# Kernel optimization log

Measured on AMD Instinct MI355X. Metric: run time of the kernel, lower is better.

The kernel has to match this reference:

```python
import jax, jax.numpy as jnp
import numpy as np

T, B, E, H, V = 512, 64, 512, 1024, 256


def setup_inputs() -> dict:
    key = jax.random.key(0)
    ks = jax.random.split(key, 10)
    s = lambda k, shape, sc: jax.random.normal(k, shape, dtype=jnp.float32) * sc
    return {
        "ints": jax.random.randint(ks[0], (T, B), 0, V),
        "encodings": s(ks[1], (V, E), 1.0),
        "output0": s(ks[2], (H,), 1.0),
        "memory0": s(ks[3], (H,), 1.0),
        "W_ih": s(ks[4], (4 * H, E), 0.03),
        "W_hh": s(ks[5], (4 * H, H), 0.03),
        "b_ih": s(ks[6], (4 * H,), 0.03),
        "b_hh": s(ks[7], (4 * H,), 0.03),
        "W_dec": s(ks[8], (V, H), 0.03),
        "b_dec": jnp.zeros((V,), dtype=jnp.float32),
    }


def reference(ints, encodings, output0, memory0, W_ih, W_hh, b_ih, b_hh, W_dec, b_dec):
    t, b = ints.shape
    h = output0.shape[0]
    x = encodings[ints]                                   # [T,B,E] embedding gather
    h0 = jnp.broadcast_to(output0, (b, h))                # learned initial hidden
    c0 = jnp.broadcast_to(memory0, (b, h))                # learned initial cell
    # precompute input projection for all timesteps (one big GEMM)
    x_proj = jnp.einsum('tbe,ge->tbg', x, W_ih) + b_ih + b_hh  # [T,B,4H]

    def step(carry, xp):
        hh, cc = carry
        gates = xp + hh @ W_hh.T                          # [B,4H]
        i, f, g, o = jnp.split(gates, 4, axis=-1)         # torch gate order i,f,g,o
        i = jax.nn.sigmoid(i)
        f = jax.nn.sigmoid(f)
        g = jnp.tanh(g)
        o = jax.nn.sigmoid(o)
        cc = f * cc + i * g
        hh = o * jnp.tanh(cc)
        return (hh, cc), hh

    _, hs = jax.lax.scan(step, (h0, c0), x_proj)          # [T,B,H]
    # outputs shifted right by one: predict char t from state after chars <t
    outs = jnp.concatenate([h0[None], hs[:-1]], axis=0)   # [T,B,H]
    return outs @ W_dec.T + b_dec                          # [T,B,V]
```

## Files before the change

kernel.cpp:

```cpp
#include <hip/hip_runtime.h>


#define TT 512
#define BB 64
#define HH 1024
#define VV 256
#define EE 512
#define SPIN_CAP 16384

typedef __attribute__((ext_vector_type(8))) short bf16x8;
typedef __attribute__((ext_vector_type(4))) float f32x4;
typedef __attribute__((ext_vector_type(4))) int i32x4;
typedef __attribute__((ext_vector_type(4))) unsigned short u16x4;

static __device__ __forceinline__ unsigned short f2bf(float f) {
  union { float f; unsigned u; } x; x.f = f;
  unsigned r = x.u + 0x7fffu + ((x.u >> 16) & 1u);
  return (unsigned short)(r >> 16);
}

__global__ void cvt_bf16(const float* __restrict__ s, unsigned short* __restrict__ d, int n4) {
  int i = blockIdx.x * blockDim.x + threadIdx.x;
  int st = gridDim.x * blockDim.x;
  for (; i < n4; i += st) {
    f32x4 v = *(const f32x4*)(s + 4l * i);
    u16x4 o;
    o.x = f2bf(v.x); o.y = f2bf(v.y); o.z = f2bf(v.z); o.w = f2bf(v.w);
    *(u16x4*)(d + 4l * i) = o;
  }
}

__global__ __launch_bounds__(256) void proj_kernel(
    const unsigned short* __restrict__ A,
    const unsigned short* __restrict__ Wi,
    const float* __restrict__ bih, const float* __restrict__ bhh,
    float* __restrict__ proj)
{
  __shared__ __align__(16) unsigned char Asm[64 * 128];
  const int tid = threadIdx.x;
  const int w = tid >> 6;
  const int lane = tid & 63;
  const int ln = lane & 15, kg = lane >> 4;
  const int m0 = blockIdx.x * 64;
  const int nb = blockIdx.y * 256 + w * 64;
  const int srow = tid >> 2, skq = tid & 3;

  f32x4 acc[4][4];
  for (int a = 0; a < 4; ++a) for (int b = 0; b < 4; ++b) acc[a][b] = (f32x4){0.f,0.f,0.f,0.f};

  for (int kc = 0; kc < 8; ++kc) {
    {
      const unsigned short* src = A + (m0 + srow) * 512 + kc * 64 + skq * 16;
      unsigned base = (unsigned)(srow * 128 + skq * 32);
      unsigned sw = (unsigned)((srow & 7) << 4);
      *(i32x4*)(Asm + ((base) ^ sw))      = *(const i32x4*)(src);
      *(i32x4*)(Asm + ((base + 16) ^ sw)) = *(const i32x4*)(src + 8);
    }
    __syncthreads();
    for (int kk = 0; kk < 2; ++kk) {
      bf16x8 afr[4];
      for (int mi = 0; mi < 4; ++mi) {
        int row = mi * 16 + ln;
        unsigned off = (unsigned)(row * 128 + (kk * 32 + kg * 8) * 2);
        afr[mi] = *(const bf16x8*)(Asm + (off ^ ((unsigned)(row & 7) << 4)));
      }
      for (int ni = 0; ni < 4; ++ni) {
        const unsigned short* bp = Wi + (nb + ni * 16 + ln) * 512 + kc * 64 + kk * 32 + kg * 8;
        bf16x8 bfr = *(const bf16x8*)bp;
        for (int mi = 0; mi < 4; ++mi)
          acc[mi][ni] = __builtin_amdgcn_mfma_f32_16x16x32_bf16(afr[mi], bfr, acc[mi][ni], 0, 0, 0);
      }
    }
    __syncthreads();
  }
  for (int ni = 0; ni < 4; ++ni) {
    int nn = nb + ni * 16 + ln;
    int gi = nn >> 10, uu = nn & 1023;
    float bias = bih[nn] + bhh[nn];
    for (int mi = 0; mi < 4; ++mi) {
      int mr = m0 + mi * 16 + kg * 4;
      for (int r = 0; r < 4; ++r)
        proj[(size_t)(mr + r) * 4096 + uu * 4 + gi] = acc[mi][ni][r] + bias;
    }
  }
}

__global__ __launch_bounds__(512, 2) void scan_kernel(
    const unsigned short* __restrict__ Whh,
    const float* __restrict__ proj,
    const int* __restrict__ ints,
    const float* __restrict__ h0v,
    const float* __restrict__ c0v,
    unsigned int* __restrict__ hcomm,
    unsigned short* __restrict__ outs)
{
  __shared__ float gatesm[8 * 8 * 128];

  const int tid = threadIdx.x;
  const int blk = blockIdx.x;
  const int g = blk & 7, r = blk >> 3;
  const int w = tid >> 6, lane = tid & 63;
  const int ln = lane & 15, kg = lane >> 4;
  const int s = (tid & 255) >> 5, u = tid & 31;
  const int sg = g * 8 + s;
  const int ug = r * 32 + u;

  bf16x8 bw[8][4];
#pragma unroll
  for (int nt = 0; nt < 8; ++nt) {
    int lrow = nt * 16 + ln;
    int grow = (lrow >> 5) * 1024 + r * 32 + (lrow & 31);
    const unsigned short* wp = Whh + (size_t)grow * 1024 + w * 128 + kg * 8;
#pragma unroll
    for (int kt = 0; kt < 4; ++kt)
      bw[nt][kt] = *(const bf16x8*)(wp + kt * 32);
  }
#pragma unroll
  for (int nt = 0; nt < 8; ++nt)
#pragma unroll
    for (int kt = 0; kt < 4; ++kt)
      asm volatile("" : "+v"(bw[nt][kt]));

  float c = (tid < 256) ? c0v[ug] : 0.f;

  if (tid < 256) {
    unsigned short hb = f2bf(h0v[ug]);
    unsigned word = ((unsigned)hb << 16) | 1u;
    unsigned* hp = hcomm + 65536 + (size_t)sg * 1024 + ug;
    asm volatile("global_store_dword %0, %1, off sc0 sc1" :: "v"(hp), "v"(word) : "memory");
    outs[(size_t)sg * 1024 + ug] = hb;
  }

  i32x4 q[8];
#pragma unroll
  for (int i = 0; i < 8; ++i) q[i] = (i32x4){0, 0, 0, 0};

  for (int t = 0; t < TT - 1; ++t) {
    f32x4 prv = (f32x4){0.f,0.f,0.f,0.f};
    if (tid < 256) {
      int vocab = ints[t * 64 + sg];
      const float* pp = proj + (size_t)vocab * 4096 + ug * 4;
      asm volatile("global_load_dwordx4 %0, %1, off" : "=v"(prv) : "v"(pp) : "memory");
    }

    const unsigned* ab = hcomm + ((size_t)((t + 1) & 1)) * 65536
                       + (size_t)(g * 8 + (ln & 7)) * 1024 + w * 128 + kg * 8;
    unsigned tgt = (unsigned)(t + 1);
    {
      int guard = 0;
      while (true) {
        if (ln < 8) {
#define LQ(i, off_lit) \
          asm volatile("global_load_dwordx4 %0, %1, off offset:" off_lit " sc0 sc1" \
                       : "=v"(q[i]) : "v"(ab) : "memory")
          LQ(0, "0");   LQ(1, "16");  LQ(2, "128"); LQ(3, "144");
          LQ(4, "256"); LQ(5, "272"); LQ(6, "384"); LQ(7, "400");
#undef LQ
        }
        asm volatile("s_waitcnt vmcnt(0)" ::: "memory");
        __builtin_amdgcn_sched_barrier(0);
        unsigned bad = 0;
        if (ln < 8) {
#pragma unroll
          for (int i = 0; i < 8; ++i) {
            bad |= ((unsigned)q[i].x ^ tgt);
            bad |= ((unsigned)q[i].y ^ tgt);
            bad |= ((unsigned)q[i].z ^ tgt);
            bad |= ((unsigned)q[i].w ^ tgt);
          }
        }
        if (__all(ln >= 8 || (bad & 0xffffu) == 0u)) break;
        if (++guard > SPIN_CAP) break;
      }
    }
    __builtin_amdgcn_sched_barrier(0);

    f32x4 acc[8];
#pragma unroll
    for (int i = 0; i < 8; ++i) acc[i] = (f32x4){0.f,0.f,0.f,0.f};
#pragma unroll
    for (int kt = 0; kt < 4; ++kt) {
      i32x4 lo = q[2 * kt], hi = q[2 * kt + 1];
      unsigned d0 = ((unsigned)lo.x >> 16) | ((unsigned)lo.y & 0xffff0000u);
      unsigned d1 = ((unsigned)lo.z >> 16) | ((unsigned)lo.w & 0xffff0000u);
      unsigned d2 = ((unsigned)hi.x >> 16) | ((unsigned)hi.y & 0xffff0000u);
      unsigned d3 = ((unsigned)hi.z >> 16) | ((unsigned)hi.w & 0xffff0000u);
      union { i32x4 i; bf16x8 h; } u2;
      u2.i = (i32x4){ (int)d0, (int)d1, (int)d2, (int)d3 };
#pragma unroll
      for (int nt = 0; nt < 8; ++nt)
        acc[nt] = __builtin_amdgcn_mfma_f32_16x16x32_bf16(u2.h, bw[nt][kt], acc[nt], 0, 0, 0);
    }

#pragma unroll
    for (int nt = 0; nt < 8; ++nt) {
      if (kg < 2) {
#pragma unroll
        for (int rr = 0; rr < 4; ++rr)
          gatesm[(w * 8 + kg * 4 + rr) * 128 + nt * 16 + ln] = acc[nt][rr];
      }
    }
    __syncthreads();

    if (tid < 256) {
      float g0 = prv.x, g1 = prv.y, g2 = prv.z, g3 = prv.w;
#pragma unroll
      for (int ww = 0; ww < 8; ++ww) {
        const float* gm = gatesm + (ww * 8 + s) * 128 + u;
        g0 += gm[0];
        g1 += gm[32];
        g2 += gm[64];
        g3 += gm[96];
      }
      float ii = __builtin_amdgcn_rcpf(1.f + __expf(-g0));
      float ff = __builtin_amdgcn_rcpf(1.f + __expf(-g1));
      float gt = 1.f - 2.f * __builtin_amdgcn_rcpf(1.f + __expf(2.f * g2));
      float oo = __builtin_amdgcn_rcpf(1.f + __expf(-g3));
      c = ff * c + ii * gt;
      float hv = oo * (1.f - 2.f * __builtin_amdgcn_rcpf(1.f + __expf(2.f * c)));

      unsigned short hb = f2bf(hv);
      unsigned word = ((unsigned)hb << 16) | ((unsigned)(t + 2) & 0xffffu);
      unsigned* hp = hcomm + ((size_t)((t + 2) & 1)) * 65536 + (size_t)sg * 1024 + ug;
      asm volatile("global_store_dword %0, %1, off sc0 sc1" :: "v"(hp), "v"(word) : "memory");
      outs[(size_t)(t + 1) * 65536 + (size_t)sg * 1024 + ug] = hb;
    }
    __syncthreads();
  }
}

__global__ __launch_bounds__(256) void decode_kernel(
    const unsigned short* __restrict__ A,
    const unsigned short* __restrict__ Wd,
    const float* __restrict__ bdec,
    float* __restrict__ out)
{
  __shared__ __align__(16) unsigned char Asm[64 * 128];
  const int tid = threadIdx.x;
  const int w = tid >> 6;
  const int lane = tid & 63;
  const int ln = lane & 15, kg = lane >> 4;
  const int m0 = blockIdx.x * 64;
  const int nb = w * 64;
  const int srow = tid >> 2, skq = tid & 3;

  f32x4 acc[4][4];
  for (int a = 0; a < 4; ++a) for (int b = 0; b < 4; ++b) acc[a][b] = (f32x4){0.f,0.f,0.f,0.f};

  for (int kc = 0; kc < 16; ++kc) {
    {
      const unsigned short* src = A + (m0 + srow) * 1024 + kc * 64 + skq * 16;
      unsigned base = (unsigned)(srow * 128 + skq * 32);
      unsigned sw = (unsigned)((srow & 7) << 4);
      *(i32x4*)(Asm + ((base) ^ sw))      = *(const i32x4*)(src);
      *(i32x4*)(Asm + ((base + 16) ^ sw)) = *(const i32x4*)(src + 8);
    }
    __syncthreads();
    for (int kk = 0; kk < 2; ++kk) {
      bf16x8 afr[4];
      for (int mi = 0; mi < 4; ++mi) {
        int row = mi * 16 + ln;
        unsigned off = (unsigned)(row * 128 + (kk * 32 + kg * 8) * 2);
        afr[mi] = *(const bf16x8*)(Asm + (off ^ ((unsigned)(row & 7) << 4)));
      }
      for (int ni = 0; ni < 4; ++ni) {
        const unsigned short* bp = Wd + (nb + ni * 16 + ln) * 1024 + kc * 64 + kk * 32 + kg * 8;
        bf16x8 bfr = *(const bf16x8*)bp;
        for (int mi = 0; mi < 4; ++mi)
          acc[mi][ni] = __builtin_amdgcn_mfma_f32_16x16x32_bf16(afr[mi], bfr, acc[mi][ni], 0, 0, 0);
      }
    }
    __syncthreads();
  }
  for (int ni = 0; ni < 4; ++ni) {
    int nn = nb + ni * 16 + ln;
    float bd = bdec[nn];
    for (int mi = 0; mi < 4; ++mi) {
      int mr = m0 + mi * 16 + kg * 4;
      for (int r = 0; r < 4; ++r)
        out[(mr + r) * 256 + nn] = acc[mi][ni][r] + bd;
    }
  }
}

extern "C" void kernel_launch(void* const* d_in, const int* in_sizes, int n_in,
                              void* d_out, int out_size, void* d_ws, size_t ws_size,
                              hipStream_t stream) {
  const int*   ints = (const int*)  d_in[0];
  const float* enc  = (const float*)d_in[1];
  const float* out0 = (const float*)d_in[2];
  const float* mem0 = (const float*)d_in[3];
  const float* Wih  = (const float*)d_in[4];
  const float* Whh  = (const float*)d_in[5];
  const float* bih  = (const float*)d_in[6];
  const float* bhh  = (const float*)d_in[7];
  const float* Wdec = (const float*)d_in[8];
  const float* bdec = (const float*)d_in[9];
  float* out = (float*)d_out;

  char* ws = (char*)d_ws;
  size_t off = 0;
  auto alloc = [&](size_t bytes) { char* p = ws + off; off += (bytes + 255) & ~(size_t)255; return p; };
  unsigned short* Whh_bf  = (unsigned short*)alloc(4096ull * 1024 * 2);
  unsigned short* enc_bf  = (unsigned short*)alloc(256ull * 512 * 2);
  unsigned short* Wih_bf  = (unsigned short*)alloc(4096ull * 512 * 2);
  unsigned short* Wdec_bf = (unsigned short*)alloc(256ull * 1024 * 2);
  float*          proj    = (float*)alloc(256ull * 4096 * 4);
  unsigned short* outs_bf = (unsigned short*)alloc(512ull * 64 * 1024 * 2);
  unsigned int*   hcomm   = (unsigned int*)alloc(2ull * 64 * 1024 * 4);

  hipMemsetAsync(hcomm, 0, 2ull * 64 * 1024 * 4, stream);

  cvt_bf16<<<512, 256, 0, stream>>>(Whh,  Whh_bf,  4096 * 1024 / 4);
  cvt_bf16<<<64,  256, 0, stream>>>(enc,  enc_bf,  256 * 512 / 4);
  cvt_bf16<<<256, 256, 0, stream>>>(Wih,  Wih_bf,  4096 * 512 / 4);
  cvt_bf16<<<64,  256, 0, stream>>>(Wdec, Wdec_bf, 256 * 1024 / 4);

  proj_kernel<<<dim3(4, 16), 256, 0, stream>>>(enc_bf, Wih_bf, bih, bhh, proj);

  {
    const unsigned short* a0 = Whh_bf;
    const float* a1 = proj;
    const int* a2 = ints;
    const float* a3 = out0;
    const float* a4 = mem0;
    unsigned int* a5 = hcomm;
    unsigned short* a6 = outs_bf;
    void* args[] = { &a0, &a1, &a2, &a3, &a4, &a5, &a6 };
    hipError_t e = hipLaunchCooperativeKernel((const void*)scan_kernel,
                                              dim3(256), dim3(512), args, 0, stream);
    if (e != hipSuccess) {
      scan_kernel<<<256, 512, 0, stream>>>(Whh_bf, proj, ints, out0, mem0,
                                           hcomm, outs_bf);
    }
  }

  decode_kernel<<<512, 256, 0, stream>>>(outs_bf, Wdec_bf, bdec, out);
}
```

Before: 1.710 ms.

## Replace per-element tagged handoff with per-step group counters and direct bf16 reads

Each block now publishes its new hidden state as plain bf16 directly into the outs buffer, then bumps a per-timestep, per-batch-group atomic counter. Consumers spin on a single counter until it reaches 32 producers, instead of polling 16-bit tags packed into every hidden element. After that they load the bf16 rows directly as MFMA operands, so the unpacking work goes away. The next step's projection load is prefetched early and the W_hh fragments are hinted into AGPRs. In exchange, each step adds a store drain and a barrier before the atomic, a second round trip after the flag, and a lower spin cap that raises the risk of silent early exits.

```diff
diff --git a/kernel.cpp b/kernel.cpp
--- a/kernel.cpp
+++ b/kernel.cpp
@@ -6,7 +6,7 @@
 #define HH 1024
 #define VV 256
 #define EE 512
-#define SPIN_CAP 16384
+#define SPIN_CAP 4096
 
 typedef __attribute__((ext_vector_type(8))) short bf16x8;
 typedef __attribute__((ext_vector_type(4))) float f32x4;
@@ -91,7 +91,7 @@
     const int* __restrict__ ints,
     const float* __restrict__ h0v,
     const float* __restrict__ c0v,
-    unsigned int* __restrict__ hcomm,
+    unsigned int* __restrict__ cnt,
     unsigned short* __restrict__ outs)
 {
   __shared__ float gatesm[8 * 8 * 128];
@@ -119,78 +119,56 @@
   for (int nt = 0; nt < 8; ++nt)
 #pragma unroll
     for (int kt = 0; kt < 4; ++kt)
-      asm volatile("" : "+v"(bw[nt][kt]));
+      asm volatile("" : "+a"(bw[nt][kt]));
 
   float c = (tid < 256) ? c0v[ug] : 0.f;
 
   if (tid < 256) {
     unsigned short hb = f2bf(h0v[ug]);
-    unsigned word = ((unsigned)hb << 16) | 1u;
-    unsigned* hp = hcomm + 65536 + (size_t)sg * 1024 + ug;
-    asm volatile("global_store_dword %0, %1, off sc0 sc1" :: "v"(hp), "v"(word) : "memory");
-    outs[(size_t)sg * 1024 + ug] = hb;
-  }
-
-  i32x4 q[8];
-#pragma unroll
-  for (int i = 0; i < 8; ++i) q[i] = (i32x4){0, 0, 0, 0};
+    unsigned short* hp = outs + (size_t)sg * 1024 + ug;
+    asm volatile("global_store_short %0, %1, off sc0 sc1" :: "v"(hp), "v"((unsigned)hb) : "memory");
+  }
+  asm volatile("s_waitcnt vmcnt(0)" ::: "memory");
+  __syncthreads();
+  if (tid == 0)
+    __hip_atomic_fetch_add(&cnt[g], 1u, __ATOMIC_RELAXED, __HIP_MEMORY_SCOPE_AGENT);
+
+  f32x4 prv = (f32x4){0.f,0.f,0.f,0.f};
+  if (tid < 256) {
+    int vocab = ints[sg];
+    prv = *(const f32x4*)(proj + (size_t)vocab * 4096 + ug * 4);
+  }
 
   for (int t = 0; t < TT - 1; ++t) {
-    f32x4 prv = (f32x4){0.f,0.f,0.f,0.f};
-    if (tid < 256) {
-      int vocab = ints[t * 64 + sg];
-      const float* pp = proj + (size_t)vocab * 4096 + ug * 4;
-      asm volatile("global_load_dwordx4 %0, %1, off" : "=v"(prv) : "v"(pp) : "memory");
-    }
-
-    const unsigned* ab = hcomm + ((size_t)((t + 1) & 1)) * 65536
-                       + (size_t)(g * 8 + (ln & 7)) * 1024 + w * 128 + kg * 8;
-    unsigned tgt = (unsigned)(t + 1);
     {
       int guard = 0;
-      while (true) {
-        if (ln < 8) {
-#define LQ(i, off_lit) \
-          asm volatile("global_load_dwordx4 %0, %1, off offset:" off_lit " sc0 sc1" \
-                       : "=v"(q[i]) : "v"(ab) : "memory")
-          LQ(0, "0");   LQ(1, "16");  LQ(2, "128"); LQ(3, "144");
-          LQ(4, "256"); LQ(5, "272"); LQ(6, "384"); LQ(7, "400");
-#undef LQ
-        }
-        asm volatile("s_waitcnt vmcnt(0)" ::: "memory");
-        __builtin_amdgcn_sched_barrier(0);
-        unsigned bad = 0;
-        if (ln < 8) {
-#pragma unroll
-          for (int i = 0; i < 8; ++i) {
-            bad |= ((unsigned)q[i].x ^ tgt);
-            bad |= ((unsigned)q[i].y ^ tgt);
-            bad |= ((unsigned)q[i].z ^ tgt);
-            bad |= ((unsigned)q[i].w ^ tgt);
-          }
-        }
-        if (__all(ln >= 8 || (bad & 0xffffu) == 0u)) break;
+      while (__hip_atomic_load(&cnt[t * 8 + g], __ATOMIC_RELAXED, __HIP_MEMORY_SCOPE_AGENT) < 32u) {
         if (++guard > SPIN_CAP) break;
       }
     }
     __builtin_amdgcn_sched_barrier(0);
 
+    bf16x8 av[4];
+    {
+      const unsigned short* ab = outs + (size_t)(t * 64 + g * 8 + (ln & 7)) * 1024
+                               + w * 128 + kg * 8;
+#define LA(i, off_lit) \
+      asm volatile("global_load_dwordx4 %0, %1, off offset:" off_lit " sc0 sc1" \
+                   : "=v"(av[i]) : "v"(ab) : "memory")
+      LA(0, "0"); LA(1, "64"); LA(2, "128"); LA(3, "192");
+#undef LA
+      asm volatile("s_waitcnt vmcnt(0)" ::: "memory");
+      __builtin_amdgcn_sched_barrier(0);
+    }
+
     f32x4 acc[8];
 #pragma unroll
     for (int i = 0; i < 8; ++i) acc[i] = (f32x4){0.f,0.f,0.f,0.f};
 #pragma unroll
-    for (int kt = 0; kt < 4; ++kt) {
-      i32x4 lo = q[2 * kt], hi = q[2 * kt + 1];
-      unsigned d0 = ((unsigned)lo.x >> 16) | ((unsigned)lo.y & 0xffff0000u);
-      unsigned d1 = ((unsigned)lo.z >> 16) | ((unsigned)lo.w & 0xffff0000u);
-      unsigned d2 = ((unsigned)hi.x >> 16) | ((unsigned)hi.y & 0xffff0000u);
-      unsigned d3 = ((unsigned)hi.z >> 16) | ((unsigned)hi.w & 0xffff0000u);
-      union { i32x4 i; bf16x8 h; } u2;
-      u2.i = (i32x4){ (int)d0, (int)d1, (int)d2, (int)d3 };
+    for (int kt = 0; kt < 4; ++kt)
 #pragma unroll
       for (int nt = 0; nt < 8; ++nt)
-        acc[nt] = __builtin_amdgcn_mfma_f32_16x16x32_bf16(u2.h, bw[nt][kt], acc[nt], 0, 0, 0);
-    }
+        acc[nt] = __builtin_amdgcn_mfma_f32_16x16x32_bf16(av[kt], bw[nt][kt], acc[nt], 0, 0, 0);
 
 #pragma unroll
     for (int nt = 0; nt < 8; ++nt) {
@@ -220,12 +198,18 @@
       float hv = oo * (1.f - 2.f * __builtin_amdgcn_rcpf(1.f + __expf(2.f * c)));
 
       unsigned short hb = f2bf(hv);
-      unsigned word = ((unsigned)hb << 16) | ((unsigned)(t + 2) & 0xffffu);
-      unsigned* hp = hcomm + ((size_t)((t + 2) & 1)) * 65536 + (size_t)sg * 1024 + ug;
-      asm volatile("global_store_dword %0, %1, off sc0 sc1" :: "v"(hp), "v"(word) : "memory");
-      outs[(size_t)(t + 1) * 65536 + (size_t)sg * 1024 + ug] = hb;
-    }
-    __syncthreads();
+      unsigned short* hp = outs + (size_t)((t + 1) * 64 + sg) * 1024 + ug;
+      asm volatile("global_store_short %0, %1, off sc0 sc1" :: "v"(hp), "v"((unsigned)hb) : "memory");
+
+      if (t + 1 < TT - 1) {
+        int vocab = ints[(t + 1) * 64 + sg];
+        prv = *(const f32x4*)(proj + (size_t)vocab * 4096 + ug * 4);
+      }
+    }
+    asm volatile("s_waitcnt vmcnt(0)" ::: "memory");
+    __syncthreads();
+    if (tid == 0)
+      __hip_atomic_fetch_add(&cnt[(t + 1) * 8 + g], 1u, __ATOMIC_RELAXED, __HIP_MEMORY_SCOPE_AGENT);
   }
 }
 
@@ -307,9 +291,9 @@
   unsigned short* Wdec_bf = (unsigned short*)alloc(256ull * 1024 * 2);
   float*          proj    = (float*)alloc(256ull * 4096 * 4);
   unsigned short* outs_bf = (unsigned short*)alloc(512ull * 64 * 1024 * 2);
-  unsigned int*   hcomm   = (unsigned int*)alloc(2ull * 64 * 1024 * 4);
-
-  hipMemsetAsync(hcomm, 0, 2ull * 64 * 1024 * 4, stream);
+  unsigned int*   cnt     = (unsigned int*)alloc(512ull * 8 * 4);
+
+  hipMemsetAsync(cnt, 0, 512ull * 8 * 4, stream);
 
   cvt_bf16<<<512, 256, 0, stream>>>(Whh,  Whh_bf,  4096 * 1024 / 4);
   cvt_bf16<<<64,  256, 0, stream>>>(enc,  enc_bf,  256 * 512 / 4);
@@ -324,14 +308,14 @@
     const int* a2 = ints;
     const float* a3 = out0;
     const float* a4 = mem0;
-    unsigned int* a5 = hcomm;
+    unsigned int* a5 = cnt;
     unsigned short* a6 = outs_bf;
     void* args[] = { &a0, &a1, &a2, &a3, &a4, &a5, &a6 };
     hipError_t e = hipLaunchCooperativeKernel((const void*)scan_kernel,
                                               dim3(256), dim3(512), args, 0, stream);
     if (e != hipSuccess) {
       scan_kernel<<<256, 512, 0, stream>>>(Whh_bf, proj, ints, out0, mem0,
-                                           hcomm, outs_bf);
+                                           cnt, outs_bf);
     }
   }
 
```

Measured after the change: 2.358 ms. +37.9%, slower.

## Remap scan blocks by XCD and use L2-local flags for intra-group sync

Applied to the files above, without the earlier changes.

Each block reads its hardware XCC ID and takes a rank within that die, so each 8-sequence group g is served by blocks on a single XCD. A rehearsal handshake then runs a number of steps using sc0-only (non-system-scope) flag loads and stores. If all 32 blocks of a group complete it without hitting the spin cap, the main scan uses L2-local sc0 accesses instead of sc0 sc1 for the hidden-state exchange. This aims to cut inter-step synchronization latency, at the cost of the startup rehearsal and reliance on hardware block placement. The W_hh fragment register pin also changes from VGPR to AGPR.

```diff
diff --git a/kernel.cpp b/kernel.cpp
--- a/kernel.cpp
+++ b/kernel.cpp
@@ -7,6 +7,8 @@
 #define VV 256
 #define EE 512
 #define SPIN_CAP 16384
+#define REH_STEPS 48
+#define REH_CAP 4096
 
 typedef __attribute__((ext_vector_type(8))) short bf16x8;
 typedef __attribute__((ext_vector_type(4))) float f32x4;
@@ -85,41 +87,18 @@
   }
 }
 
-__global__ __launch_bounds__(512, 2) void scan_kernel(
-    const unsigned short* __restrict__ Whh,
-    const float* __restrict__ proj,
-    const int* __restrict__ ints,
-    const float* __restrict__ h0v,
-    const float* __restrict__ c0v,
-    unsigned int* __restrict__ hcomm,
-    unsigned short* __restrict__ outs)
+template<bool LOCAL>
+static __device__ __forceinline__ void scan_loop(
+    int g, int r, int tid, bf16x8 (&bw)[8][4],
+    const float* __restrict__ proj, const int* __restrict__ ints,
+    const float* __restrict__ h0v, const float* __restrict__ c0v,
+    unsigned int* __restrict__ hcomm, unsigned short* __restrict__ outs,
+    float* gatesm)
 {
-  __shared__ float gatesm[8 * 8 * 128];
-
-  const int tid = threadIdx.x;
-  const int blk = blockIdx.x;
-  const int g = blk & 7, r = blk >> 3;
   const int w = tid >> 6, lane = tid & 63;
   const int ln = lane & 15, kg = lane >> 4;
   const int s = (tid & 255) >> 5, u = tid & 31;
-  const int sg = g * 8 + s;
-  const int ug = r * 32 + u;
-
-  bf16x8 bw[8][4];
-#pragma unroll
-  for (int nt = 0; nt < 8; ++nt) {
-    int lrow = nt * 16 + ln;
-    int grow = (lrow >> 5) * 1024 + r * 32 + (lrow & 31);
-    const unsigned short* wp = Whh + (size_t)grow * 1024 + w * 128 + kg * 8;
-#pragma unroll
-    for (int kt = 0; kt < 4; ++kt)
-      bw[nt][kt] = *(const bf16x8*)(wp + kt * 32);
-  }
-#pragma unroll
-  for (int nt = 0; nt < 8; ++nt)
-#pragma unroll
-    for (int kt = 0; kt < 4; ++kt)
-      asm volatile("" : "+v"(bw[nt][kt]));
+  const int sg = g * 8 + s, ug = r * 32 + u;
 
   float c = (tid < 256) ? c0v[ug] : 0.f;
 
@@ -127,7 +106,8 @@
     unsigned short hb = f2bf(h0v[ug]);
     unsigned word = ((unsigned)hb << 16) | 1u;
     unsigned* hp = hcomm + 65536 + (size_t)sg * 1024 + ug;
-    asm volatile("global_store_dword %0, %1, off sc0 sc1" :: "v"(hp), "v"(word) : "memory");
+    if (LOCAL) asm volatile("global_store_dword %0, %1, off sc0"     :: "v"(hp), "v"(word) : "memory");
+    else       asm volatile("global_store_dword %0, %1, off sc0 sc1" :: "v"(hp), "v"(word) : "memory");
     outs[(size_t)sg * 1024 + ug] = hb;
   }
 
@@ -150,12 +130,21 @@
       int guard = 0;
       while (true) {
         if (ln < 8) {
-#define LQ(i, off_lit) \
+#define LQL(i, off_lit) \
+          asm volatile("global_load_dwordx4 %0, %1, off offset:" off_lit " sc0" \
+                       : "=v"(q[i]) : "v"(ab) : "memory")
+#define LQG(i, off_lit) \
           asm volatile("global_load_dwordx4 %0, %1, off offset:" off_lit " sc0 sc1" \
                        : "=v"(q[i]) : "v"(ab) : "memory")
-          LQ(0, "0");   LQ(1, "16");  LQ(2, "128"); LQ(3, "144");
-          LQ(4, "256"); LQ(5, "272"); LQ(6, "384"); LQ(7, "400");
-#undef LQ
+          if (LOCAL) {
+            LQL(0, "0");   LQL(1, "16");  LQL(2, "128"); LQL(3, "144");
+            LQL(4, "256"); LQL(5, "272"); LQL(6, "384"); LQL(7, "400");
+          } else {
+            LQG(0, "0");   LQG(1, "16");  LQG(2, "128"); LQG(3, "144");
+            LQG(4, "256"); LQG(5, "272"); LQG(6, "384"); LQG(7, "400");
+          }
+#undef LQL
+#undef LQG
         }
         asm volatile("s_waitcnt vmcnt(0)" ::: "memory");
         __builtin_amdgcn_sched_barrier(0);
@@ -222,11 +211,170 @@
       unsigned short hb = f2bf(hv);
       unsigned word = ((unsigned)hb << 16) | ((unsigned)(t + 2) & 0xffffu);
       unsigned* hp = hcomm + ((size_t)((t + 2) & 1)) * 65536 + (size_t)sg * 1024 + ug;
-      asm volatile("global_store_dword %0, %1, off sc0 sc1" :: "v"(hp), "v"(word) : "memory");
+      if (LOCAL) asm volatile("global_store_dword %0, %1, off sc0"     :: "v"(hp), "v"(word) : "memory");
+      else       asm volatile("global_store_dword %0, %1, off sc0 sc1" :: "v"(hp), "v"(word) : "memory");
       outs[(size_t)(t + 1) * 65536 + (size_t)sg * 1024 + ug] = hb;
     }
     __syncthreads();
   }
+}
+
+__global__ __launch_bounds__(512, 2) void scan_kernel(
+    const unsigned short* __restrict__ Whh,
+    const float* __restrict__ proj,
+    const int* __restrict__ ints,
+    const float* __restrict__ h0v,
+    const float* __restrict__ c0v,
+    unsigned int* __restrict__ hcomm,
+    unsigned int* __restrict__ rhbuf,
+    unsigned int* __restrict__ ctrl,
+    unsigned short* __restrict__ outs)
+{
+  __shared__ float gatesm[8 * 8 * 128];
+  __shared__ int s_g, s_r, s_bal, s_fail, s_mode;
+
+  const int tid = threadIdx.x;
+  const int blk = blockIdx.x;
+
+  if (tid == 0) {
+    unsigned xcd;
+    asm volatile("s_getreg_b32 %0, hwreg(HW_REG_XCC_ID)" : "=s"(xcd));
+    xcd &= 7u;
+    unsigned rank = __hip_atomic_fetch_add(&ctrl[xcd], 1u, __ATOMIC_RELAXED,
+                                           __HIP_MEMORY_SCOPE_AGENT);
+    __hip_atomic_fetch_add(&ctrl[8], 1u, __ATOMIC_RELEASE, __HIP_MEMORY_SCOPE_AGENT);
+    int guard = 0;
+    while (__hip_atomic_load(&ctrl[8], __ATOMIC_ACQUIRE, __HIP_MEMORY_SCOPE_AGENT) < 256u)
+      if (++guard > (1 << 20)) break;
+    unsigned bal = (rank < 32u) ? 1u : 0u;
+    for (int k = 0; k < 8; ++k)
+      bal &= (__hip_atomic_load(&ctrl[k], __ATOMIC_RELAXED, __HIP_MEMORY_SCOPE_AGENT) == 32u)
+             ? 1u : 0u;
+    s_bal = (int)bal;
+    s_g = bal ? (int)xcd  : (blk & 7);
+    s_r = bal ? (int)rank : (blk >> 3);
+    s_fail = 0;
+    s_mode = 0;
+  }
+  __syncthreads();
+  const int g = s_g, r = s_r;
+  const int w = tid >> 6, lane = tid & 63;
+  const int ln = lane & 15, kg = lane >> 4;
+  const int s = (tid & 255) >> 5, u = tid & 31;
+  const int sg = g * 8 + s, ug = r * 32 + u;
+
+  bf16x8 bw[8][4];
+#pragma unroll
+  for (int nt = 0; nt < 8; ++nt) {
+    int lrow = nt * 16 + ln;
+    int grow = (lrow >> 5) * 1024 + r * 32 + (lrow & 31);
+    const unsigned short* wp = Whh + (size_t)grow * 1024 + w * 128 + kg * 8;
+#pragma unroll
+    for (int kt = 0; kt < 4; ++kt)
+      bw[nt][kt] = *(const bf16x8*)(wp + kt * 32);
+  }
+#pragma unroll
+  for (int nt = 0; nt < 8; ++nt)
+#pragma unroll
+    for (int kt = 0; kt < 4; ++kt)
+      asm volatile("" : "+a"(bw[nt][kt]));
+
+  if (s_bal) {
+    if (tid < 256) {
+      unsigned* p0 = rhbuf + (size_t)sg * 1024 + ug;
+      unsigned* p1 = rhbuf + 65536 + (size_t)sg * 1024 + ug;
+      unsigned z = 0;
+      asm volatile("global_store_dword %0, %1, off sc0" :: "v"(p0), "v"(z) : "memory");
+      asm volatile("global_store_dword %0, %1, off sc0" :: "v"(p1), "v"(z) : "memory");
+    }
+    asm volatile("s_waitcnt vmcnt(0)" ::: "memory");
+    __syncthreads();
+    if (tid < 256) {
+      unsigned word = 1u;
+      unsigned* hp = rhbuf + 65536 + (size_t)sg * 1024 + ug;
+      asm volatile("global_store_dword %0, %1, off sc0" :: "v"(hp), "v"(word) : "memory");
+    }
+    for (int t = 0; t < REH_STEPS - 1; ++t) {
+      const unsigned* ab = rhbuf + ((size_t)((t + 1) & 1)) * 65536
+                         + (size_t)(g * 8 + (ln & 7)) * 1024 + w * 128 + kg * 8;
+      unsigned tgt = (unsigned)(t + 1);
+      i32x4 q2[8];
+#pragma unroll
+      for (int i = 0; i < 8; ++i) q2[i] = (i32x4){0, 0, 0, 0};
+      int already = __hip_atomic_load(&s_fail, __ATOMIC_RELAXED, __HIP_MEMORY_SCOPE_WORKGROUP);
+      if (!already) {
+        int guard = 0;
+        while (true) {
+          if (ln < 8) {
+#define LR(i, off_lit) \
+            asm volatile("global_load_dwordx4 %0, %1, off offset:" off_lit " sc0" \
+                         : "=v"(q2[i]) : "v"(ab) : "memory")
+            LR(0, "0");   LR(1, "16");  LR(2, "128"); LR(3, "144");
+            LR(4, "256"); LR(5, "272"); LR(6, "384"); LR(7, "400");
+#undef LR
+          }
+          asm volatile("s_waitcnt vmcnt(0)" ::: "memory");
+          __builtin_amdgcn_sched_barrier(0);
+          unsigned bad = 0;
+          if (ln < 8) {
+#pragma unroll
+            for (int i = 0; i < 8; ++i) {
+              bad |= ((unsigned)q2[i].x ^ tgt);
+              bad |= ((unsigned)q2[i].y ^ tgt);
+              bad |= ((unsigned)q2[i].z ^ tgt);
+              bad |= ((unsigned)q2[i].w ^ tgt);
+            }
+          }
+          if (__all(ln >= 8 || (bad & 0xffffu) == 0u)) break;
+          if (++guard > REH_CAP) {
+            if (lane == 0)
+              __hip_atomic_store(&s_fail, 1, __ATOMIC_RELAXED, __HIP_MEMORY_SCOPE_WORKGROUP);
+            break;
+          }
+        }
+      }
+      __syncthreads();
+      if (tid < 256) {
+        unsigned word = (unsigned)(t + 2);
+        unsigned* hp = rhbuf + ((size_t)((t + 2) & 1)) * 65536 + (size_t)sg * 1024 + ug;
+        asm volatile("global_store_dword %0, %1, off sc0" :: "v"(hp), "v"(word) : "memory");
+      }
+      __syncthreads();
+    }
+    __syncthreads();
+
+    if (tid < 256) {
+      unsigned* p0 = hcomm + (size_t)sg * 1024 + ug;
+      unsigned* p1 = hcomm + 65536 + (size_t)sg * 1024 + ug;
+      unsigned z = 0;
+      asm volatile("global_store_dword %0, %1, off sc0" :: "v"(p0), "v"(z) : "memory");
+      asm volatile("global_store_dword %0, %1, off sc0" :: "v"(p1), "v"(z) : "memory");
+    }
+    asm volatile("s_waitcnt vmcnt(0)" ::: "memory");
+    __syncthreads();
+
+    int ok = (__hip_atomic_load(&s_fail, __ATOMIC_RELAXED, __HIP_MEMORY_SCOPE_WORKGROUP) == 0);
+    if (tid == 0)
+      __hip_atomic_store(&ctrl[16 + g * 32 + r], ok ? 2u : 1u,
+                         __ATOMIC_RELAXED, __HIP_MEMORY_SCOPE_AGENT);
+    if (tid == 0) s_mode = 1;
+    __syncthreads();
+    if (tid < 32) {
+      unsigned v = 0;
+      int guard = 0;
+      while ((v = __hip_atomic_load(&ctrl[16 + g * 32 + tid], __ATOMIC_RELAXED,
+                                    __HIP_MEMORY_SCOPE_AGENT)) == 0u)
+        if (++guard > (1 << 20)) break;
+      if (v != 2u)
+        __hip_atomic_store(&s_mode, 0, __ATOMIC_RELAXED, __HIP_MEMORY_SCOPE_WORKGROUP);
+    }
+    __syncthreads();
+  }
+
+  if (s_mode)
+    scan_loop<true >(g, r, tid, bw, proj, ints, h0v, c0v, hcomm, outs, gatesm);
+  else
+    scan_loop<false>(g, r, tid, bw, proj, ints, h0v, c0v, hcomm, outs, gatesm);
 }
 
 __global__ __launch_bounds__(256) void decode_kernel(
@@ -308,8 +456,10 @@
   float*          proj    = (float*)alloc(256ull * 4096 * 4);
   unsigned short* outs_bf = (unsigned short*)alloc(512ull * 64 * 1024 * 2);
   unsigned int*   hcomm   = (unsigned int*)alloc(2ull * 64 * 1024 * 4);
-
-  hipMemsetAsync(hcomm, 0, 2ull * 64 * 1024 * 4, stream);
+  unsigned int*   rhbuf   = (unsigned int*)alloc(2ull * 64 * 1024 * 4);
+  unsigned int*   ctrl    = (unsigned int*)alloc(272 * 4);
+
+  hipMemsetAsync(hcomm, 0, 2ull * (2ull * 64 * 1024 * 4 + 256) + 272 * 4, stream);
 
   cvt_bf16<<<512, 256, 0, stream>>>(Whh,  Whh_bf,  4096 * 1024 / 4);
   cvt_bf16<<<64,  256, 0, stream>>>(enc,  enc_bf,  256 * 512 / 4);
@@ -325,13 +475,15 @@
     const float* a3 = out0;
     const float* a4 = mem0;
     unsigned int* a5 = hcomm;
-    unsigned short* a6 = outs_bf;
-    void* args[] = { &a0, &a1, &a2, &a3, &a4, &a5, &a6 };
+    unsigned int* a6 = rhbuf;
+    unsigned int* a7 = ctrl;
+    unsigned short* a8 = outs_bf;
+    void* args[] = { &a0, &a1, &a2, &a3, &a4, &a5, &a6, &a7, &a8 };
     hipError_t e = hipLaunchCooperativeKernel((const void*)scan_kernel,
                                               dim3(256), dim3(512), args, 0, stream);
     if (e != hipSuccess) {
       scan_kernel<<<256, 512, 0, stream>>>(Whh_bf, proj, ints, out0, mem0,
-                                           hcomm, outs_bf);
+                                           hcomm, rhbuf, ctrl, outs_bf);
     }
   }
 
```

New measurement: 6.259 ms. 3.66x slower.

## Poll hidden-state chunks per k-tile and double-buffer gate smem to drop barrier

Applied to the files above, without the earlier changes.

The spin-wait on the flag-tagged hidden-state buffer is split into four per-k-tile polls, so MFMA work on early chunks can start before the whole slice is ready. The gate scratch buffer in LDS is double-buffered by timestep parity, which lets the trailing __syncthreads per step be removed. The register-resident W_hh fragments are also pinned to AGPRs to ease VGPR pressure. The costs are more polling round trips per step and twice the LDS footprint, which may reduce occupancy.

```diff
diff --git a/kernel.cpp b/kernel.cpp
--- a/kernel.cpp
+++ b/kernel.cpp
@@ -94,7 +94,7 @@
     unsigned int* __restrict__ hcomm,
     unsigned short* __restrict__ outs)
 {
-  __shared__ float gatesm[8 * 8 * 128];
+  __shared__ float gatesm[2 * 8 * 8 * 128];
 
   const int tid = threadIdx.x;
   const int blk = blockIdx.x;
@@ -119,7 +119,7 @@
   for (int nt = 0; nt < 8; ++nt)
 #pragma unroll
     for (int kt = 0; kt < 4; ++kt)
-      asm volatile("" : "+v"(bw[nt][kt]));
+      asm volatile("" : "+a"(bw[nt][kt]));
 
   float c = (tid < 256) ? c0v[ug] : 0.f;
 
@@ -131,10 +131,6 @@
     outs[(size_t)sg * 1024 + ug] = hb;
   }
 
-  i32x4 q[8];
-#pragma unroll
-  for (int i = 0; i < 8; ++i) q[i] = (i32x4){0, 0, 0, 0};
-
   for (int t = 0; t < TT - 1; ++t) {
     f32x4 prv = (f32x4){0.f,0.f,0.f,0.f};
     if (tid < 256) {
@@ -146,45 +142,41 @@
     const unsigned* ab = hcomm + ((size_t)((t + 1) & 1)) * 65536
                        + (size_t)(g * 8 + (ln & 7)) * 1024 + w * 128 + kg * 8;
     unsigned tgt = (unsigned)(t + 1);
-    {
-      int guard = 0;
-      while (true) {
-        if (ln < 8) {
-#define LQ(i, off_lit) \
-          asm volatile("global_load_dwordx4 %0, %1, off offset:" off_lit " sc0 sc1" \
-                       : "=v"(q[i]) : "v"(ab) : "memory")
-          LQ(0, "0");   LQ(1, "16");  LQ(2, "128"); LQ(3, "144");
-          LQ(4, "256"); LQ(5, "272"); LQ(6, "384"); LQ(7, "400");
-#undef LQ
+    f32x4 acc[8];
+#pragma unroll
+    for (int i = 0; i < 8; ++i) acc[i] = (f32x4){0.f,0.f,0.f,0.f};
+
+#pragma unroll
+    for (int kt = 0; kt < 4; ++kt) {
+      i32x4 qa = (i32x4){0,0,0,0}, qb = (i32x4){0,0,0,0};
+      {
+        const unsigned* abk = ab + kt * 32;
+        int guard = 0;
+        while (true) {
+          if (ln < 8) {
+            asm volatile("global_load_dwordx4 %0, %1, off sc0 sc1"
+                         : "=v"(qa) : "v"(abk) : "memory");
+            asm volatile("global_load_dwordx4 %0, %1, off offset:16 sc0 sc1"
+                         : "=v"(qb) : "v"(abk) : "memory");
+          }
+          asm volatile("s_waitcnt vmcnt(0)" ::: "memory");
+          __builtin_amdgcn_sched_barrier(0);
+          unsigned bad = 0;
+          if (ln < 8) {
+            bad |= ((unsigned)qa.x ^ tgt); bad |= ((unsigned)qa.y ^ tgt);
+            bad |= ((unsigned)qa.z ^ tgt); bad |= ((unsigned)qa.w ^ tgt);
+            bad |= ((unsigned)qb.x ^ tgt); bad |= ((unsigned)qb.y ^ tgt);
+            bad |= ((unsigned)qb.z ^ tgt); bad |= ((unsigned)qb.w ^ tgt);
+          }
+          if (__all(ln >= 8 || (bad & 0xffffu) == 0u)) break;
+          if (++guard > SPIN_CAP) break;
         }
-        asm volatile("s_waitcnt vmcnt(0)" ::: "memory");
-        __builtin_amdgcn_sched_barrier(0);
-        unsigned bad = 0;
-        if (ln < 8) {
-#pragma unroll
-          for (int i = 0; i < 8; ++i) {
-            bad |= ((unsigned)q[i].x ^ tgt);
-            bad |= ((unsigned)q[i].y ^ tgt);
-            bad |= ((unsigned)q[i].z ^ tgt);
-            bad |= ((unsigned)q[i].w ^ tgt);
-          }
-        }
-        if (__all(ln >= 8 || (bad & 0xffffu) == 0u)) break;
-        if (++guard > SPIN_CAP) break;
-      }
-    }
-    __builtin_amdgcn_sched_barrier(0);
-
-    f32x4 acc[8];
-#pragma unroll
-    for (int i = 0; i < 8; ++i) acc[i] = (f32x4){0.f,0.f,0.f,0.f};
-#pragma unroll
-    for (int kt = 0; kt < 4; ++kt) {
-      i32x4 lo = q[2 * kt], hi = q[2 * kt + 1];
-      unsigned d0 = ((unsigned)lo.x >> 16) | ((unsigned)lo.y & 0xffff0000u);
-      unsigned d1 = ((unsigned)lo.z >> 16) | ((unsigned)lo.w & 0xffff0000u);
-      unsigned d2 = ((unsigned)hi.x >> 16) | ((unsigned)hi.y & 0xffff0000u);
-      unsigned d3 = ((unsigned)hi.z >> 16) | ((unsigned)hi.w & 0xffff0000u);
+      }
+      __builtin_amdgcn_sched_barrier(0);
+      unsigned d0 = ((unsigned)qa.x >> 16) | ((unsigned)qa.y & 0xffff0000u);
+      unsigned d1 = ((unsigned)qa.z >> 16) | ((unsigned)qa.w & 0xffff0000u);
+      unsigned d2 = ((unsigned)qb.x >> 16) | ((unsigned)qb.y & 0xffff0000u);
+      unsigned d3 = ((unsigned)qb.z >> 16) | ((unsigned)qb.w & 0xffff0000u);
       union { i32x4 i; bf16x8 h; } u2;
       u2.i = (i32x4){ (int)d0, (int)d1, (int)d2, (int)d3 };
 #pragma unroll
@@ -192,12 +184,13 @@
         acc[nt] = __builtin_amdgcn_mfma_f32_16x16x32_bf16(u2.h, bw[nt][kt], acc[nt], 0, 0, 0);
     }
 
+    float* gm0 = gatesm + (t & 1) * 8192;
 #pragma unroll
     for (int nt = 0; nt < 8; ++nt) {
       if (kg < 2) {
 #pragma unroll
         for (int rr = 0; rr < 4; ++rr)
-          gatesm[(w * 8 + kg * 4 + rr) * 128 + nt * 16 + ln] = acc[nt][rr];
+          gm0[(w * 8 + kg * 4 + rr) * 128 + nt * 16 + ln] = acc[nt][rr];
       }
     }
     __syncthreads();
@@ -206,11 +199,11 @@
       float g0 = prv.x, g1 = prv.y, g2 = prv.z, g3 = prv.w;
 #pragma unroll
       for (int ww = 0; ww < 8; ++ww) {
-        const float* gm = gatesm + (ww * 8 + s) * 128 + u;
-        g0 += gm[0];
-        g1 += gm[32];
-        g2 += gm[64];
-        g3 += gm[96];
+        const float* gp = gm0 + (ww * 8 + s) * 128 + u;
+        g0 += gp[0];
+        g1 += gp[32];
+        g2 += gp[64];
+        g3 += gp[96];
       }
       float ii = __builtin_amdgcn_rcpf(1.f + __expf(-g0));
       float ff = __builtin_amdgcn_rcpf(1.f + __expf(-g1));
@@ -225,7 +218,6 @@
       asm volatile("global_store_dword %0, %1, off sc0 sc1" :: "v"(hp), "v"(word) : "memory");
       outs[(size_t)(t + 1) * 65536 + (size_t)sg * 1024 + ug] = hb;
     }
-    __syncthreads();
   }
 }
 
```

After: 1.928 ms. 12.8% more time.
